# Performance work log

Measured on AMD Instinct MI355X. Metric: run time of the kernel, lower is better.

## Reference

```python
import jax, jax.numpy as jnp
import numpy as np

B, E, S, H = 4, 1024, 2048, 16  # batch, dim, seq_len, n_heads


def setup_inputs() -> dict:
    key = jax.random.key(0)
    ks = jax.random.split(key, 7)
    x = jax.random.normal(ks[0], (B, E, S), dtype=jnp.float32)
    in_w = jax.random.normal(ks[1], (E, E), dtype=jnp.float32) * (1.0 / np.sqrt(E))
    in_b = jnp.zeros((E,), dtype=jnp.float32)
    out_w = jax.random.normal(ks[2], (E, E), dtype=jnp.float32) * (1.0 / np.sqrt(E))
    out_b = jnp.zeros((E,), dtype=jnp.float32)
    mix_w = jax.random.normal(ks[3], (H, S), dtype=jnp.float32)
    mix_b = jnp.zeros((H, S), dtype=jnp.float32)
    return {"x": x, "in_w": in_w, "in_b": in_b, "out_w": out_w,
            "out_b": out_b, "mix_w": mix_w, "mix_b": mix_b}


def _head_matrices(mix_w):
    # First H/2 heads: column-repeat causal M[i,j] = v[j] if j >= i else 0.
    # Last  H/2 heads: row-repeat causal    M[i,j] = v[i] if j >= i else 0.
    idx = jnp.arange(S)
    mask = idx[None, :] >= idx[:, None]  # (S, S), True where j >= i
    Wcol = jnp.where(mask[None], mix_w[: H // 2, None, :], jnp.zeros((), mix_w.dtype))
    Wrow = jnp.where(mask[None], mix_w[H // 2 :, :, None], jnp.zeros((), mix_w.dtype))
    return jnp.concatenate([Wcol, Wrow], axis=0)  # (H, S, S)


def reference(x, in_w, in_b, out_w, out_b, mix_w, mix_b):
    e = E // H  # per-head channel dim
    xt = jnp.transpose(x, (0, 2, 1))           # b t e
    xt = xt @ in_w.T + in_b                    # in_proj
    # 'b t (h e) -> b h e t'
    p = jnp.transpose(xt.reshape(B, S, H, e), (0, 2, 3, 1))
    Wm = _head_matrices(mix_w)                 # (H, S, S)
    # bmm per (batch, head): (e, S) @ (S, S)
    out = jnp.einsum('bhet,hts->bhes', p, Wm) + mix_b[None, :, None, :]
    # 'b h e t -> b t (h e)'
    out = jnp.transpose(out, (0, 3, 1, 2)).reshape(B, S, E)
    out = out @ out_w.T + out_b                # out_proj
    return jnp.transpose(out, (0, 2, 1))       # b e t
```

## Files before the change

### kernel.cpp

```cpp
#include <hip/hip_runtime.h>

#define B_ 4
#define E_ 1024
#define S_ 2048
#define H_ 16
#define K_ 1024

#define NCH 32
#define CS  (S_/NCH)

typedef __bf16 bf16x8 __attribute__((ext_vector_type(8)));
typedef float  f32x4  __attribute__((ext_vector_type(4)));

#define AS1 __attribute__((address_space(1)))
#define AS3 __attribute__((address_space(3)))

__device__ __forceinline__ unsigned short f2bf(float f) {
  unsigned u = __float_as_uint(f);
  u += 0x7fffu + ((u >> 16) & 1u);
  return (unsigned short)(u >> 16);
}
__device__ __forceinline__ float bf2f(unsigned short h) {
  return __uint_as_float(((unsigned)h) << 16);
}

__global__ __launch_bounds__(256)
void tc_kernel(const float* __restrict__ x, unsigned short* __restrict__ xt,
               const float* __restrict__ inw, const float* __restrict__ outw,
               unsigned short* __restrict__ w1, unsigned short* __restrict__ w2)
{
  if (blockIdx.z == 4) {
    const int per = (E_ * E_) / 4;
    const int fid = blockIdx.y * 32 + blockIdx.x;
#pragma unroll
    for (int k = 0; k < 4; ++k) {
      int i = fid * 1024 + k * 256 + threadIdx.x;
      const float4* src = (i < per) ? (const float4*)inw : (const float4*)outw;
      unsigned short* dst = (i < per) ? w1 : w2;
      int j = (i < per) ? i : i - per;
      float4 v = src[j];
      ushort4 o;
      o.x = f2bf(v.x); o.y = f2bf(v.y); o.z = f2bf(v.z); o.w = f2bf(v.w);
      *(ushort4*)(dst + (long)j * 4) = o;
    }
    return;
  }

  __shared__ float t[64][65];
  const int b  = blockIdx.z;
  const int e0 = blockIdx.y * 64;
  const int s0 = blockIdx.x * 64;
  const int tx = threadIdx.x & 63, ty = threadIdx.x >> 6;

  const float* xp = x + ((long)b * E_ + e0) * S_ + s0;
#pragma unroll
  for (int r = 0; r < 16; ++r) {
    int row = r * 4 + ty;
    t[row][tx] = xp[(long)row * S_ + tx];
  }
  __syncthreads();
  unsigned short* xo = xt + ((long)b * S_ + s0) * E_ + e0;
#pragma unroll
  for (int p = 0; p < 2; ++p) {
    int s = p * 32 + (threadIdx.x >> 3);
    int e = (threadIdx.x & 7) * 8;
    unsigned short v[8];
#pragma unroll
    for (int j = 0; j < 8; ++j) v[j] = f2bf(t[e + j][s]);
    *(ushort4*)(xo + (long)s * E_ + e)     = make_ushort4(v[0], v[1], v[2], v[3]);
    *(ushort4*)(xo + (long)s * E_ + e + 4) = make_ushort4(v[4], v[5], v[6], v[7]);
  }
}

__device__ __forceinline__ void stage_half(char* lds, const unsigned short* __restrict__ base,
                                           int kt, int ks, int tid) {
  int row = tid >> 2;
  int cb  = (tid & 3) << 4;
  int cbs = cb ^ (((row >> 1) & 3) << 4);
  const unsigned short* src = base + (long)row * K_ + kt + ks * 32 + (cbs >> 1);
  __builtin_amdgcn_global_load_lds((const AS1 void*)src,
      (AS3 void*)(lds + ks * 8192 + tid * 16), 16, 0, 0);
}

__device__ __forceinline__ void stage_tile(char* buf, const unsigned short* __restrict__ Ab,
                                           const unsigned short* __restrict__ Bb,
                                           int kt, int tid) {
  stage_half(buf,         Ab, kt, 0, tid);
  stage_half(buf,         Ab, kt, 1, tid);
  stage_half(buf + 16384, Bb, kt, 0, tid);
  stage_half(buf + 16384, Bb, kt, 1, tid);
}

template<int VARIANT>
__global__ __launch_bounds__(512, 4)
void gemm_hw(const unsigned short* __restrict__ A, const unsigned short* __restrict__ Bw,
             void* __restrict__ Cout, const float* __restrict__ bias,
             const float* __restrict__ mixw, float* __restrict__ part)
{
  __shared__ char smem[65536];

  const int tid  = threadIdx.x;
  const int lane = tid & 63, wid = tid >> 6;
  const int wm = wid >> 2, wn = wid & 3;
  const int lr = lane & 15, lg = lane >> 4;

  const int bid = blockIdx.x;
  const int xcd = bid & 7;
  const int j   = bid >> 3;
  const int tm  = (xcd << 3) | (j & 7);
  const int tn  = j >> 3;

  const unsigned short* Ab = A  + (long)tm * 128 * K_;
  const unsigned short* Bb = Bw + (long)tn * 128 * K_;

  f32x4 acc[4][2] = {};

  stage_tile(smem, Ab, Bb, 0, tid);
  __syncthreads();

  for (int t = 0; t < 16; ++t) {
    char* cur = smem + (t & 1) * 32768;
    char* nxt = smem + ((t + 1) & 1) * 32768;
    if (t + 1 < 16) stage_tile(nxt, Ab, Bb, (t + 1) * 64, tid);

#pragma unroll
    for (int ks = 0; ks < 2; ++ks) {
      bf16x8 af[4], bfv[2];
#pragma unroll
      for (int mf = 0; mf < 4; ++mf) {
        int row = wm * 64 + mf * 16 + lr;
        int cb  = (lg * 16) ^ (((row >> 1) & 3) << 4);
        af[mf] = *(const bf16x8*)(cur + ks * 8192 + row * 64 + cb);
      }
#pragma unroll
      for (int nf = 0; nf < 2; ++nf) {
        int row = wn * 32 + nf * 16 + lr;
        int cb  = (lg * 16) ^ (((row >> 1) & 3) << 4);
        bfv[nf] = *(const bf16x8*)(cur + 16384 + ks * 8192 + row * 64 + cb);
      }
#pragma unroll
      for (int mf = 0; mf < 4; ++mf)
#pragma unroll
        for (int nf = 0; nf < 2; ++nf)
          acc[mf][nf] = __builtin_amdgcn_mfma_f32_16x16x32_bf16(
              af[mf], bfv[nf], acc[mf][nf], 0, 0, 0);
    }
    __syncthreads();
  }

  if constexpr (VARIANT == 0) {
    const int bt = tm >> 4;
    const int sb = ((tm & 15) << 7) + wm * 64;
    const int ch = ((tm & 15) << 1) + wm;
#pragma unroll
    for (int nf = 0; nf < 2; ++nf) {
      const int c = tn * 128 + wn * 32 + nf * 16 + lr;
      const float bv = bias[c];
      const int h = c >> 6;
      float sm = 0.f;
#pragma unroll
      for (int mf = 0; mf < 4; ++mf) {
#pragma unroll
        for (int jj = 0; jj < 4; ++jj) {
          const int sl = sb + mf * 16 + lg * 4 + jj;
          float v = acc[mf][nf][jj] + bv;
          ((unsigned short*)Cout)[((long)bt * S_ + sl) * E_ + c] = f2bf(v);
          sm += (h < 8) ? v : v * mixw[h * S_ + sl];
        }
      }
      sm += __shfl_xor(sm, 16, 64);
      sm += __shfl_xor(sm, 32, 64);
      if (lg == 0) part[((long)bt * NCH + ch) * E_ + c] = sm;
    }
  } else {
#pragma unroll
    for (int nf = 0; nf < 2; ++nf) {
      const int c = tn * 128 + wn * 32 + nf * 16 + lr;
      const float bv = bias[c];
#pragma unroll
      for (int mf = 0; mf < 4; ++mf) {
        const int r0 = tm * 128 + wm * 64 + mf * 16 + lg * 4;
        const int s = r0 & (S_ - 1);
        const int b = r0 >> 11;
        float4 v;
        v.x = acc[mf][nf][0] + bv; v.y = acc[mf][nf][1] + bv;
        v.z = acc[mf][nf][2] + bv; v.w = acc[mf][nf][3] + bv;
        *(float4*)((float*)Cout + ((long)b * E_ + c) * S_ + s) = v;
      }
    }
  }
}

__global__ __launch_bounds__(256)
void scan_final(const unsigned short* __restrict__ yt, const float* __restrict__ mixw,
                const float* __restrict__ mixb, const float* __restrict__ part,
                unsigned short* __restrict__ zt)
{
  const int b  = blockIdx.z;
  const int c  = blockIdx.y * 256 + threadIdx.x;
  const int ch = blockIdx.x;
  const int h  = c >> 6;
  float acc = 0.f;
  for (int p = 0; p < ch; ++p) acc += part[((long)b * NCH + p) * E_ + c];
  const unsigned short* yp = yt + ((long)b * S_ + ch * CS) * E_ + c;
  unsigned short*       zp = zt + ((long)b * S_ + ch * CS) * E_ + c;
  const float* mw = mixw + (long)h * S_ + ch * CS;
  const float* mb = mixb + (long)h * S_ + ch * CS;
  if (h < 8) {
    for (int s = 0; s < CS; ++s) {
      acc += bf2f(yp[(long)s * E_]);
      zp[(long)s * E_] = f2bf(fmaf(acc, mw[s], mb[s]));
    }
  } else {
    for (int s = 0; s < CS; ++s) {
      acc += bf2f(yp[(long)s * E_]) * mw[s];
      zp[(long)s * E_] = f2bf(acc + mb[s]);
    }
  }
}

extern "C" void kernel_launch(void* const* d_in, const int* in_sizes, int n_in,
                              void* d_out, int out_size, void* d_ws, size_t ws_size,
                              hipStream_t stream)
{
  (void)in_sizes; (void)n_in; (void)out_size; (void)ws_size;
  const float* x     = (const float*)d_in[0];
  const float* in_w  = (const float*)d_in[1];
  const float* in_b  = (const float*)d_in[2];
  const float* out_w = (const float*)d_in[3];
  const float* out_b = (const float*)d_in[4];
  const float* mix_w = (const float*)d_in[5];
  const float* mix_b = (const float*)d_in[6];

  char* ws = (char*)d_ws;
  unsigned short* Xt  = (unsigned short*)(ws);
  unsigned short* Yt  = (unsigned short*)(ws + (size_t)16 * 1024 * 1024);
  unsigned short* W1b = (unsigned short*)(ws + (size_t)32 * 1024 * 1024);
  unsigned short* W2b = (unsigned short*)(ws + (size_t)34 * 1024 * 1024);
  float*          part = (float*)(ws + (size_t)36 * 1024 * 1024);
  unsigned short* Zt  = Xt;

  tc_kernel<<<dim3(S_ / 64, E_ / 64, 5), 256, 0, stream>>>(x, Xt, in_w, out_w, W1b, W2b);

  gemm_hw<0><<<dim3(512), 512, 0, stream>>>(Xt, W1b, Yt, in_b, mix_w, part);

  scan_final<<<dim3(NCH, E_ / 256, B_), 256, 0, stream>>>(Yt, mix_w, mix_b, part, Zt);

  gemm_hw<1><<<dim3(512), 512, 0, stream>>>(Zt, W2b, d_out, out_b, nullptr, nullptr);
}
```

Before: 77.51 us.

## Fuse input transpose and fp32-to-bf16 conversion into GEMM tile staging

```diff
diff --git a/kernel.cpp b/kernel.cpp
--- a/kernel.cpp
+++ b/kernel.cpp
@@ -11,9 +11,11 @@
 
 typedef __bf16 bf16x8 __attribute__((ext_vector_type(8)));
 typedef float  f32x4  __attribute__((ext_vector_type(4)));
+typedef unsigned short u16x8 __attribute__((ext_vector_type(8)));
 
 #define AS1 __attribute__((address_space(1)))
 #define AS3 __attribute__((address_space(3)))
+#define SWZ(row) ((((row) >> 1) & 3) << 4)
 
 __device__ __forceinline__ unsigned short f2bf(float f) {
   unsigned u = __float_as_uint(f);
@@ -24,119 +26,92 @@
   return __uint_as_float(((unsigned)h) << 16);
 }
 
-__global__ __launch_bounds__(256)
-void tc_kernel(const float* __restrict__ x, unsigned short* __restrict__ xt,
-               const float* __restrict__ inw, const float* __restrict__ outw,
-               unsigned short* __restrict__ w1, unsigned short* __restrict__ w2)
-{
-  if (blockIdx.z == 4) {
-    const int per = (E_ * E_) / 4;
-    const int fid = blockIdx.y * 32 + blockIdx.x;
-#pragma unroll
-    for (int k = 0; k < 4; ++k) {
-      int i = fid * 1024 + k * 256 + threadIdx.x;
-      const float4* src = (i < per) ? (const float4*)inw : (const float4*)outw;
-      unsigned short* dst = (i < per) ? w1 : w2;
-      int j = (i < per) ? i : i - per;
-      float4 v = src[j];
-      ushort4 o;
-      o.x = f2bf(v.x); o.y = f2bf(v.y); o.z = f2bf(v.z); o.w = f2bf(v.w);
-      *(ushort4*)(dst + (long)j * 4) = o;
-    }
-    return;
-  }
-
-  __shared__ float t[64][65];
-  const int b  = blockIdx.z;
-  const int e0 = blockIdx.y * 64;
-  const int s0 = blockIdx.x * 64;
-  const int tx = threadIdx.x & 63, ty = threadIdx.x >> 6;
-
-  const float* xp = x + ((long)b * E_ + e0) * S_ + s0;
-#pragma unroll
-  for (int r = 0; r < 16; ++r) {
-    int row = r * 4 + ty;
-    t[row][tx] = xp[(long)row * S_ + tx];
-  }
-  __syncthreads();
-  unsigned short* xo = xt + ((long)b * S_ + s0) * E_ + e0;
-#pragma unroll
-  for (int p = 0; p < 2; ++p) {
-    int s = p * 32 + (threadIdx.x >> 3);
-    int e = (threadIdx.x & 7) * 8;
-    unsigned short v[8];
-#pragma unroll
-    for (int j = 0; j < 8; ++j) v[j] = f2bf(t[e + j][s]);
-    *(ushort4*)(xo + (long)s * E_ + e)     = make_ushort4(v[0], v[1], v[2], v[3]);
-    *(ushort4*)(xo + (long)s * E_ + e + 4) = make_ushort4(v[4], v[5], v[6], v[7]);
-  }
-}
-
-__device__ __forceinline__ void stage_half(char* lds, const unsigned short* __restrict__ base,
-                                           int kt, int ks, int tid) {
-  int row = tid >> 2;
-  int cb  = (tid & 3) << 4;
-  int cbs = cb ^ (((row >> 1) & 3) << 4);
-  const unsigned short* src = base + (long)row * K_ + kt + ks * 32 + (cbs >> 1);
-  __builtin_amdgcn_global_load_lds((const AS1 void*)src,
-      (AS3 void*)(lds + ks * 8192 + tid * 16), 16, 0, 0);
-}
-
-__device__ __forceinline__ void stage_tile(char* buf, const unsigned short* __restrict__ Ab,
-                                           const unsigned short* __restrict__ Bb,
-                                           int kt, int tid) {
-  stage_half(buf,         Ab, kt, 0, tid);
-  stage_half(buf,         Ab, kt, 1, tid);
-  stage_half(buf + 16384, Bb, kt, 0, tid);
-  stage_half(buf + 16384, Bb, kt, 1, tid);
-}
-
-template<int VARIANT>
 __global__ __launch_bounds__(512, 4)
-void gemm_hw(const unsigned short* __restrict__ A, const unsigned short* __restrict__ Bw,
-             void* __restrict__ Cout, const float* __restrict__ bias,
-             const float* __restrict__ mixw, float* __restrict__ part)
+void gemm1_fused(const float* __restrict__ x, const float* __restrict__ W1,
+                 unsigned short* __restrict__ Yt, const float* __restrict__ bias,
+                 const float* __restrict__ mixw, float* __restrict__ part)
 {
   __shared__ char smem[65536];
-
   const int tid  = threadIdx.x;
   const int lane = tid & 63, wid = tid >> 6;
   const int wm = wid >> 2, wn = wid & 3;
   const int lr = lane & 15, lg = lane >> 4;
 
   const int bid = blockIdx.x;
-  const int xcd = bid & 7;
-  const int j   = bid >> 3;
+  const int xcd = bid & 7, j = bid >> 3;
   const int tm  = (xcd << 3) | (j & 7);
   const int tn  = j >> 3;
 
-  const unsigned short* Ab = A  + (long)tm * 128 * K_;
-  const unsigned short* Bb = Bw + (long)tn * 128 * K_;
+  const int bt  = tm >> 4;
+  const int sl0 = (tm & 15) << 7;
+
+  const int ae  = tid & 63;
+  const int asq = tid >> 6;
+  const float* xbase = x + ((long)bt * E_ + ae) * S_ + sl0 + asq * 16;
+  const int bc  = tid >> 2;
+  const int beq = tid & 3;
+  const float* wbase = W1 + (long)(tn * 128 + bc) * E_ + beq * 16;
+
+  float4 ax[4], bx[4];
+  auto loadAB = [&](int t) {
+    const float* pa = xbase + (long)t * 64 * S_;
+    const float* pb = wbase + t * 64;
+#pragma unroll
+    for (int i = 0; i < 4; ++i) ax[i] = *(const float4*)(pa + i * 4);
+#pragma unroll
+    for (int i = 0; i < 4; ++i) bx[i] = *(const float4*)(pb + i * 4);
+  };
+  auto cvtwrite = [&](char* buf) {
+#pragma unroll
+    for (int i = 0; i < 4; ++i) {
+      float v0 = ax[i].x, v1 = ax[i].y, v2 = ax[i].z, v3 = ax[i].w;
+      int half = ae >> 5, colb = (ae & 31) * 2;
+#pragma unroll
+      for (int jj = 0; jj < 4; ++jj) {
+        int srow = asq * 16 + i * 4 + jj;
+        float vv = jj == 0 ? v0 : jj == 1 ? v1 : jj == 2 ? v2 : v3;
+        *(unsigned short*)(buf + half * 8192 + srow * 64 + (colb ^ SWZ(srow))) = f2bf(vv);
+      }
+    }
+    u16x8 bv[2];
+#pragma unroll
+    for (int i = 0; i < 4; ++i) {
+      bv[i >> 1][(i & 1) * 4 + 0] = f2bf(bx[i].x);
+      bv[i >> 1][(i & 1) * 4 + 1] = f2bf(bx[i].y);
+      bv[i >> 1][(i & 1) * 4 + 2] = f2bf(bx[i].z);
+      bv[i >> 1][(i & 1) * 4 + 3] = f2bf(bx[i].w);
+    }
+    int half = beq >> 1, colb = (beq & 1) * 32;
+    int base = 16384 + half * 8192 + bc * 64;
+#pragma unroll
+    for (int u = 0; u < 2; ++u)
+      *(u16x8*)(buf + base + ((colb + u * 16) ^ SWZ(bc))) = bv[u];
+  };
 
   f32x4 acc[4][2] = {};
 
-  stage_tile(smem, Ab, Bb, 0, tid);
+  loadAB(0);
+  cvtwrite(smem);
+  loadAB(1);
   __syncthreads();
 
   for (int t = 0; t < 16; ++t) {
     char* cur = smem + (t & 1) * 32768;
     char* nxt = smem + ((t + 1) & 1) * 32768;
-    if (t + 1 < 16) stage_tile(nxt, Ab, Bb, (t + 1) * 64, tid);
-
+    if (t < 15) cvtwrite(nxt);
+    if (t < 14) loadAB(t + 2);
 #pragma unroll
     for (int ks = 0; ks < 2; ++ks) {
       bf16x8 af[4], bfv[2];
 #pragma unroll
       for (int mf = 0; mf < 4; ++mf) {
         int row = wm * 64 + mf * 16 + lr;
-        int cb  = (lg * 16) ^ (((row >> 1) & 3) << 4);
-        af[mf] = *(const bf16x8*)(cur + ks * 8192 + row * 64 + cb);
+        af[mf] = *(const bf16x8*)(cur + ks * 8192 + row * 64 + ((lg * 16) ^ SWZ(row)));
       }
 #pragma unroll
       for (int nf = 0; nf < 2; ++nf) {
         int row = wn * 32 + nf * 16 + lr;
-        int cb  = (lg * 16) ^ (((row >> 1) & 3) << 4);
-        bfv[nf] = *(const bf16x8*)(cur + 16384 + ks * 8192 + row * 64 + cb);
+        bfv[nf] = *(const bf16x8*)(cur + 16384 + ks * 8192 + row * 64 + ((lg * 16) ^ SWZ(row)));
       }
 #pragma unroll
       for (int mf = 0; mf < 4; ++mf)
@@ -148,45 +123,136 @@
     __syncthreads();
   }
 
-  if constexpr (VARIANT == 0) {
-    const int bt = tm >> 4;
-    const int sb = ((tm & 15) << 7) + wm * 64;
-    const int ch = ((tm & 15) << 1) + wm;
-#pragma unroll
-    for (int nf = 0; nf < 2; ++nf) {
-      const int c = tn * 128 + wn * 32 + nf * 16 + lr;
-      const float bv = bias[c];
-      const int h = c >> 6;
-      float sm = 0.f;
+  const int sb = sl0 + wm * 64;
+  const int ch = ((tm & 15) << 1) + wm;
+#pragma unroll
+  for (int nf = 0; nf < 2; ++nf) {
+    const int c = tn * 128 + wn * 32 + nf * 16 + lr;
+    const float bv = bias[c];
+    const int h = c >> 6;
+    float sm = 0.f;
+#pragma unroll
+    for (int mf = 0; mf < 4; ++mf) {
+#pragma unroll
+      for (int jj = 0; jj < 4; ++jj) {
+        const int sl = sb + mf * 16 + lg * 4 + jj;
+        float v = acc[mf][nf][jj] + bv;
+        Yt[((long)bt * S_ + sl) * E_ + c] = f2bf(v);
+        sm += (h < 8) ? v : v * mixw[h * S_ + sl];
+      }
+    }
+    sm += __shfl_xor(sm, 16, 64);
+    sm += __shfl_xor(sm, 32, 64);
+    if (lg == 0) part[((long)bt * NCH + ch) * E_ + c] = sm;
+  }
+}
+
+__device__ __forceinline__ void stage_halfA(char* lds, const unsigned short* __restrict__ base,
+                                            int kt, int ks, int tid) {
+  int row = tid >> 2;
+  int cb  = (tid & 3) << 4;
+  int cbs = cb ^ SWZ(row);
+  const unsigned short* src = base + (long)row * K_ + kt + ks * 32 + (cbs >> 1);
+  __builtin_amdgcn_global_load_lds((const AS1 void*)src,
+      (AS3 void*)(lds + ks * 8192 + tid * 16), 16, 0, 0);
+}
+
+__global__ __launch_bounds__(512, 4)
+void gemm2_fused(const unsigned short* __restrict__ Zt, const float* __restrict__ W2,
+                 float* __restrict__ out, const float* __restrict__ bias)
+{
+  __shared__ char smem[65536];
+  const int tid  = threadIdx.x;
+  const int lane = tid & 63, wid = tid >> 6;
+  const int wm = wid >> 2, wn = wid & 3;
+  const int lr = lane & 15, lg = lane >> 4;
+
+  const int bid = blockIdx.x;
+  const int xcd = bid & 7, j = bid >> 3;
+  const int tm  = (xcd << 3) | (j & 7);
+  const int tn  = j >> 3;
+
+  const unsigned short* Ab = Zt + (long)tm * 128 * K_;
+  const int bc  = tid >> 2;
+  const int beq = tid & 3;
+  const float* wbase = W2 + (long)(tn * 128 + bc) * E_ + beq * 16;
+
+  float4 bx[4];
+  auto loadB = [&](int t) {
+    const float* pb = wbase + t * 64;
+#pragma unroll
+    for (int i = 0; i < 4; ++i) bx[i] = *(const float4*)(pb + i * 4);
+  };
+  auto cvtwriteB = [&](char* buf) {
+    u16x8 bv[2];
+#pragma unroll
+    for (int i = 0; i < 4; ++i) {
+      bv[i >> 1][(i & 1) * 4 + 0] = f2bf(bx[i].x);
+      bv[i >> 1][(i & 1) * 4 + 1] = f2bf(bx[i].y);
+      bv[i >> 1][(i & 1) * 4 + 2] = f2bf(bx[i].z);
+      bv[i >> 1][(i & 1) * 4 + 3] = f2bf(bx[i].w);
+    }
+    int half = beq >> 1, colb = (beq & 1) * 32;
+    int base = 16384 + half * 8192 + bc * 64;
+#pragma unroll
+    for (int u = 0; u < 2; ++u)
+      *(u16x8*)(buf + base + ((colb + u * 16) ^ SWZ(bc))) = bv[u];
+  };
+
+  f32x4 acc[4][2] = {};
+
+  loadB(0);
+  stage_halfA(smem, Ab, 0, 0, tid);
+  stage_halfA(smem, Ab, 0, 1, tid);
+  cvtwriteB(smem);
+  loadB(1);
+  __syncthreads();
+
+  for (int t = 0; t < 16; ++t) {
+    char* cur = smem + (t & 1) * 32768;
+    char* nxt = smem + ((t + 1) & 1) * 32768;
+    if (t < 15) {
+      stage_halfA(nxt, Ab, (t + 1) * 64, 0, tid);
+      stage_halfA(nxt, Ab, (t + 1) * 64, 1, tid);
+      cvtwriteB(nxt);
+    }
+    if (t < 14) loadB(t + 2);
+#pragma unroll
+    for (int ks = 0; ks < 2; ++ks) {
+      bf16x8 af[4], bfv[2];
 #pragma unroll
       for (int mf = 0; mf < 4; ++mf) {
-#pragma unroll
-        for (int jj = 0; jj < 4; ++jj) {
-          const int sl = sb + mf * 16 + lg * 4 + jj;
-          float v = acc[mf][nf][jj] + bv;
-          ((unsigned short*)Cout)[((long)bt * S_ + sl) * E_ + c] = f2bf(v);
-          sm += (h < 8) ? v : v * mixw[h * S_ + sl];
-        }
-      }
-      sm += __shfl_xor(sm, 16, 64);
-      sm += __shfl_xor(sm, 32, 64);
-      if (lg == 0) part[((long)bt * NCH + ch) * E_ + c] = sm;
-    }
-  } else {
-#pragma unroll
-    for (int nf = 0; nf < 2; ++nf) {
-      const int c = tn * 128 + wn * 32 + nf * 16 + lr;
-      const float bv = bias[c];
-#pragma unroll
-      for (int mf = 0; mf < 4; ++mf) {
-        const int r0 = tm * 128 + wm * 64 + mf * 16 + lg * 4;
-        const int s = r0 & (S_ - 1);
-        const int b = r0 >> 11;
-        float4 v;
-        v.x = acc[mf][nf][0] + bv; v.y = acc[mf][nf][1] + bv;
-        v.z = acc[mf][nf][2] + bv; v.w = acc[mf][nf][3] + bv;
-        *(float4*)((float*)Cout + ((long)b * E_ + c) * S_ + s) = v;
-      }
+        int row = wm * 64 + mf * 16 + lr;
+        af[mf] = *(const bf16x8*)(cur + ks * 8192 + row * 64 + ((lg * 16) ^ SWZ(row)));
+      }
+#pragma unroll
+      for (int nf = 0; nf < 2; ++nf) {
+        int row = wn * 32 + nf * 16 + lr;
+        bfv[nf] = *(const bf16x8*)(cur + 16384 + ks * 8192 + row * 64 + ((lg * 16) ^ SWZ(row)));
+      }
+#pragma unroll
+      for (int mf = 0; mf < 4; ++mf)
+#pragma unroll
+        for (int nf = 0; nf < 2; ++nf)
+          acc[mf][nf] = __builtin_amdgcn_mfma_f32_16x16x32_bf16(
+              af[mf], bfv[nf], acc[mf][nf], 0, 0, 0);
+    }
+    __syncthreads();
+  }
+
+#pragma unroll
+  for (int nf = 0; nf < 2; ++nf) {
+    const int c = tn * 128 + wn * 32 + nf * 16 + lr;
+    const float bv = bias[c];
+#pragma unroll
+    for (int mf = 0; mf < 4; ++mf) {
+      const int r0 = tm * 128 + wm * 64 + mf * 16 + lg * 4;
+      const int s = r0 & (S_ - 1);
+      const int b = r0 >> 11;
+      float4 v;
+      v.x = acc[mf][nf][0] + bv; v.y = acc[mf][nf][1] + bv;
+      v.z = acc[mf][nf][2] + bv; v.w = acc[mf][nf][3] + bv;
+      *(float4*)(out + ((long)b * E_ + c) * S_ + s) = v;
     }
   }
 }
@@ -233,18 +299,13 @@
   const float* mix_b = (const float*)d_in[6];
 
   char* ws = (char*)d_ws;
-  unsigned short* Xt  = (unsigned short*)(ws);
-  unsigned short* Yt  = (unsigned short*)(ws + (size_t)16 * 1024 * 1024);
-  unsigned short* W1b = (unsigned short*)(ws + (size_t)32 * 1024 * 1024);
-  unsigned short* W2b = (unsigned short*)(ws + (size_t)34 * 1024 * 1024);
-  float*          part = (float*)(ws + (size_t)36 * 1024 * 1024);
-  unsigned short* Zt  = Xt;
-
-  tc_kernel<<<dim3(S_ / 64, E_ / 64, 5), 256, 0, stream>>>(x, Xt, in_w, out_w, W1b, W2b);
-
-  gemm_hw<0><<<dim3(512), 512, 0, stream>>>(Xt, W1b, Yt, in_b, mix_w, part);
+  unsigned short* Yt  = (unsigned short*)(ws);
+  unsigned short* Zt  = (unsigned short*)(ws + (size_t)16 * 1024 * 1024);
+  float*          part = (float*)(ws + (size_t)32 * 1024 * 1024);
+
+  gemm1_fused<<<dim3(512), 512, 0, stream>>>(x, in_w, Yt, in_b, mix_w, part);
 
   scan_final<<<dim3(NCH, E_ / 256, B_), 256, 0, stream>>>(Yt, mix_w, mix_b, part, Zt);
 
-  gemm_hw<1><<<dim3(512), 512, 0, stream>>>(Zt, W2b, d_out, out_b, nullptr, nullptr);
-}
+  gemm2_fused<<<dim3(512), 512, 0, stream>>>(Zt, out_w, (float*)d_out, out_b);
+}
```

After: 109.3 us. +41.0%, slower.

## Fuse fp32 weight conversion into GEMM B staging and split K across warp pairs

Applied to the files above, without the earlier changes.

```diff
diff --git a/kernel.cpp b/kernel.cpp
--- a/kernel.cpp
+++ b/kernel.cpp
@@ -11,9 +11,11 @@
 
 typedef __bf16 bf16x8 __attribute__((ext_vector_type(8)));
 typedef float  f32x4  __attribute__((ext_vector_type(4)));
+typedef unsigned short u16x8 __attribute__((ext_vector_type(8)));
 
 #define AS1 __attribute__((address_space(1)))
 #define AS3 __attribute__((address_space(3)))
+#define SWZ(row) ((((row) >> 1) & 3) << 4)
 
 __device__ __forceinline__ unsigned short f2bf(float f) {
   unsigned u = __float_as_uint(f);
@@ -25,27 +27,8 @@
 }
 
 __global__ __launch_bounds__(256)
-void tc_kernel(const float* __restrict__ x, unsigned short* __restrict__ xt,
-               const float* __restrict__ inw, const float* __restrict__ outw,
-               unsigned short* __restrict__ w1, unsigned short* __restrict__ w2)
-{
-  if (blockIdx.z == 4) {
-    const int per = (E_ * E_) / 4;
-    const int fid = blockIdx.y * 32 + blockIdx.x;
-#pragma unroll
-    for (int k = 0; k < 4; ++k) {
-      int i = fid * 1024 + k * 256 + threadIdx.x;
-      const float4* src = (i < per) ? (const float4*)inw : (const float4*)outw;
-      unsigned short* dst = (i < per) ? w1 : w2;
-      int j = (i < per) ? i : i - per;
-      float4 v = src[j];
-      ushort4 o;
-      o.x = f2bf(v.x); o.y = f2bf(v.y); o.z = f2bf(v.z); o.w = f2bf(v.w);
-      *(ushort4*)(dst + (long)j * 4) = o;
-    }
-    return;
-  }
-
+void transpose_convert(const float* __restrict__ x, unsigned short* __restrict__ xt)
+{
   __shared__ float t[64][65];
   const int b  = blockIdx.z;
   const int e0 = blockIdx.y * 64;
@@ -72,120 +55,150 @@
   }
 }
 
-__device__ __forceinline__ void stage_half(char* lds, const unsigned short* __restrict__ base,
-                                           int kt, int ks, int tid) {
+__device__ __forceinline__ void stage_halfA(char* lds, const unsigned short* __restrict__ base,
+                                            int kt, int ks, int tid) {
   int row = tid >> 2;
   int cb  = (tid & 3) << 4;
-  int cbs = cb ^ (((row >> 1) & 3) << 4);
+  int cbs = cb ^ SWZ(row);
   const unsigned short* src = base + (long)row * K_ + kt + ks * 32 + (cbs >> 1);
   __builtin_amdgcn_global_load_lds((const AS1 void*)src,
       (AS3 void*)(lds + ks * 8192 + tid * 16), 16, 0, 0);
 }
 
-__device__ __forceinline__ void stage_tile(char* buf, const unsigned short* __restrict__ Ab,
-                                           const unsigned short* __restrict__ Bb,
-                                           int kt, int tid) {
-  stage_half(buf,         Ab, kt, 0, tid);
-  stage_half(buf,         Ab, kt, 1, tid);
-  stage_half(buf + 16384, Bb, kt, 0, tid);
-  stage_half(buf + 16384, Bb, kt, 1, tid);
-}
-
 template<int VARIANT>
 __global__ __launch_bounds__(512, 4)
-void gemm_hw(const unsigned short* __restrict__ A, const unsigned short* __restrict__ Bw,
+void gemm_ks(const unsigned short* __restrict__ A, const float* __restrict__ W,
              void* __restrict__ Cout, const float* __restrict__ bias,
              const float* __restrict__ mixw, float* __restrict__ part)
 {
   __shared__ char smem[65536];
-
   const int tid  = threadIdx.x;
   const int lane = tid & 63, wid = tid >> 6;
-  const int wm = wid >> 2, wn = wid & 3;
+  const int p  = wid >> 1, g = wid & 1;
+  const int wm = p >> 1,   wn = p & 1;
   const int lr = lane & 15, lg = lane >> 4;
 
   const int bid = blockIdx.x;
-  const int xcd = bid & 7;
-  const int j   = bid >> 3;
+  const int xcd = bid & 7, j = bid >> 3;
   const int tm  = (xcd << 3) | (j & 7);
   const int tn  = j >> 3;
 
-  const unsigned short* Ab = A  + (long)tm * 128 * K_;
-  const unsigned short* Bb = Bw + (long)tn * 128 * K_;
-
-  f32x4 acc[4][2] = {};
-
-  stage_tile(smem, Ab, Bb, 0, tid);
+  const unsigned short* Ab = A + (long)tm * 128 * K_;
+  const int bc  = tid >> 2;
+  const int beq = tid & 3;
+  const float* wbase = W + (long)(tn * 128 + bc) * E_ + beq * 16;
+
+  float4 bx[4];
+  auto loadB = [&](int t) {
+    const float* pb = wbase + t * 64;
+#pragma unroll
+    for (int i = 0; i < 4; ++i) bx[i] = *(const float4*)(pb + i * 4);
+  };
+  auto cvtwriteB = [&](char* buf) {
+    u16x8 bv[2];
+#pragma unroll
+    for (int i = 0; i < 4; ++i) {
+      bv[i >> 1][(i & 1) * 4 + 0] = f2bf(bx[i].x);
+      bv[i >> 1][(i & 1) * 4 + 1] = f2bf(bx[i].y);
+      bv[i >> 1][(i & 1) * 4 + 2] = f2bf(bx[i].z);
+      bv[i >> 1][(i & 1) * 4 + 3] = f2bf(bx[i].w);
+    }
+    int half = beq >> 1, colb = (beq & 1) * 32;
+    int base = 16384 + half * 8192 + bc * 64;
+#pragma unroll
+    for (int u = 0; u < 2; ++u)
+      *(u16x8*)(buf + base + ((colb + u * 16) ^ SWZ(bc))) = bv[u];
+  };
+
+  f32x4 acc[4][4] = {};
+
+  loadB(0);
+  stage_halfA(smem, Ab, 0, 0, tid);
+  stage_halfA(smem, Ab, 0, 1, tid);
+  cvtwriteB(smem);
+  loadB(1);
   __syncthreads();
 
   for (int t = 0; t < 16; ++t) {
     char* cur = smem + (t & 1) * 32768;
     char* nxt = smem + ((t + 1) & 1) * 32768;
-    if (t + 1 < 16) stage_tile(nxt, Ab, Bb, (t + 1) * 64, tid);
-
-#pragma unroll
-    for (int ks = 0; ks < 2; ++ks) {
-      bf16x8 af[4], bfv[2];
-#pragma unroll
-      for (int mf = 0; mf < 4; ++mf) {
-        int row = wm * 64 + mf * 16 + lr;
-        int cb  = (lg * 16) ^ (((row >> 1) & 3) << 4);
-        af[mf] = *(const bf16x8*)(cur + ks * 8192 + row * 64 + cb);
+    if (t < 15) {
+      stage_halfA(nxt, Ab, (t + 1) * 64, 0, tid);
+      stage_halfA(nxt, Ab, (t + 1) * 64, 1, tid);
+      cvtwriteB(nxt);
+    }
+    if (t < 14) loadB(t + 2);
+
+    bf16x8 af[4], bfv[4];
+#pragma unroll
+    for (int mf = 0; mf < 4; ++mf) {
+      int row = wm * 64 + mf * 16 + lr;
+      af[mf] = *(const bf16x8*)(cur + g * 8192 + row * 64 + ((lg * 16) ^ SWZ(row)));
+    }
+#pragma unroll
+    for (int nf = 0; nf < 4; ++nf) {
+      int row = wn * 64 + nf * 16 + lr;
+      bfv[nf] = *(const bf16x8*)(cur + 16384 + g * 8192 + row * 64 + ((lg * 16) ^ SWZ(row)));
+    }
+#pragma unroll
+    for (int mf = 0; mf < 4; ++mf)
+#pragma unroll
+      for (int nf = 0; nf < 4; ++nf)
+        acc[mf][nf] = __builtin_amdgcn_mfma_f32_16x16x32_bf16(
+            af[mf], bfv[nf], acc[mf][nf], 0, 0, 0);
+    __syncthreads();
+  }
+
+  f32x4* xch = (f32x4*)(void*)smem + p * 1024;
+  if (g == 1) {
+#pragma unroll
+    for (int i = 0; i < 16; ++i) xch[i * 64 + lane] = acc[i >> 2][i & 3];
+  }
+  __syncthreads();
+  if (g == 0) {
+#pragma unroll
+    for (int i = 0; i < 16; ++i) acc[i >> 2][i & 3] += xch[i * 64 + lane];
+
+    if constexpr (VARIANT == 0) {
+      const int bt  = tm >> 4;
+      const int sl0 = (tm & 15) << 7;
+      const int sb  = sl0 + wm * 64;
+      const int ch  = ((tm & 15) << 1) + wm;
+#pragma unroll
+      for (int nf = 0; nf < 4; ++nf) {
+        const int c = tn * 128 + wn * 64 + nf * 16 + lr;
+        const float bv = bias[c];
+        const int h = c >> 6;
+        float sm = 0.f;
+#pragma unroll
+        for (int mf = 0; mf < 4; ++mf) {
+#pragma unroll
+          for (int jj = 0; jj < 4; ++jj) {
+            const int sl = sb + mf * 16 + lg * 4 + jj;
+            float v = acc[mf][nf][jj] + bv;
+            ((unsigned short*)Cout)[((long)bt * S_ + sl) * E_ + c] = f2bf(v);
+            sm += (h < 8) ? v : v * mixw[h * S_ + sl];
+          }
+        }
+        sm += __shfl_xor(sm, 16, 64);
+        sm += __shfl_xor(sm, 32, 64);
+        if (lg == 0) part[((long)bt * NCH + ch) * E_ + c] = sm;
       }
-#pragma unroll
-      for (int nf = 0; nf < 2; ++nf) {
-        int row = wn * 32 + nf * 16 + lr;
-        int cb  = (lg * 16) ^ (((row >> 1) & 3) << 4);
-        bfv[nf] = *(const bf16x8*)(cur + 16384 + ks * 8192 + row * 64 + cb);
-      }
-#pragma unroll
-      for (int mf = 0; mf < 4; ++mf)
-#pragma unroll
-        for (int nf = 0; nf < 2; ++nf)
-          acc[mf][nf] = __builtin_amdgcn_mfma_f32_16x16x32_bf16(
-              af[mf], bfv[nf], acc[mf][nf], 0, 0, 0);
-    }
-    __syncthreads();
-  }
-
-  if constexpr (VARIANT == 0) {
-    const int bt = tm >> 4;
-    const int sb = ((tm & 15) << 7) + wm * 64;
-    const int ch = ((tm & 15) << 1) + wm;
-#pragma unroll
-    for (int nf = 0; nf < 2; ++nf) {
-      const int c = tn * 128 + wn * 32 + nf * 16 + lr;
-      const float bv = bias[c];
-      const int h = c >> 6;
-      float sm = 0.f;
-#pragma unroll
-      for (int mf = 0; mf < 4; ++mf) {
-#pragma unroll
-        for (int jj = 0; jj < 4; ++jj) {
-          const int sl = sb + mf * 16 + lg * 4 + jj;
-          float v = acc[mf][nf][jj] + bv;
-          ((unsigned short*)Cout)[((long)bt * S_ + sl) * E_ + c] = f2bf(v);
-          sm += (h < 8) ? v : v * mixw[h * S_ + sl];
+    } else {
+#pragma unroll
+      for (int nf = 0; nf < 4; ++nf) {
+        const int c = tn * 128 + wn * 64 + nf * 16 + lr;
+        const float bv = bias[c];
+#pragma unroll
+        for (int mf = 0; mf < 4; ++mf) {
+          const int r0 = tm * 128 + wm * 64 + mf * 16 + lg * 4;
+          const int s = r0 & (S_ - 1);
+          const int b = r0 >> 11;
+          float4 v;
+          v.x = acc[mf][nf][0] + bv; v.y = acc[mf][nf][1] + bv;
+          v.z = acc[mf][nf][2] + bv; v.w = acc[mf][nf][3] + bv;
+          *(float4*)((float*)Cout + ((long)b * E_ + c) * S_ + s) = v;
         }
-      }
-      sm += __shfl_xor(sm, 16, 64);
-      sm += __shfl_xor(sm, 32, 64);
-      if (lg == 0) part[((long)bt * NCH + ch) * E_ + c] = sm;
-    }
-  } else {
-#pragma unroll
-    for (int nf = 0; nf < 2; ++nf) {
-      const int c = tn * 128 + wn * 32 + nf * 16 + lr;
-      const float bv = bias[c];
-#pragma unroll
-      for (int mf = 0; mf < 4; ++mf) {
-        const int r0 = tm * 128 + wm * 64 + mf * 16 + lg * 4;
-        const int s = r0 & (S_ - 1);
-        const int b = r0 >> 11;
-        float4 v;
-        v.x = acc[mf][nf][0] + bv; v.y = acc[mf][nf][1] + bv;
-        v.z = acc[mf][nf][2] + bv; v.w = acc[mf][nf][3] + bv;
-        *(float4*)((float*)Cout + ((long)b * E_ + c) * S_ + s) = v;
       }
     }
   }
@@ -235,16 +248,14 @@
   char* ws = (char*)d_ws;
   unsigned short* Xt  = (unsigned short*)(ws);
   unsigned short* Yt  = (unsigned short*)(ws + (size_t)16 * 1024 * 1024);
-  unsigned short* W1b = (unsigned short*)(ws + (size_t)32 * 1024 * 1024);
-  unsigned short* W2b = (unsigned short*)(ws + (size_t)34 * 1024 * 1024);
-  float*          part = (float*)(ws + (size_t)36 * 1024 * 1024);
+  float*          part = (float*)(ws + (size_t)32 * 1024 * 1024);
   unsigned short* Zt  = Xt;
 
-  tc_kernel<<<dim3(S_ / 64, E_ / 64, 5), 256, 0, stream>>>(x, Xt, in_w, out_w, W1b, W2b);
-
-  gemm_hw<0><<<dim3(512), 512, 0, stream>>>(Xt, W1b, Yt, in_b, mix_w, part);
+  transpose_convert<<<dim3(S_ / 64, E_ / 64, B_), 256, 0, stream>>>(x, Xt);
+
+  gemm_ks<0><<<dim3(512), 512, 0, stream>>>(Xt, in_w, Yt, in_b, mix_w, part);
 
   scan_final<<<dim3(NCH, E_ / 256, B_), 256, 0, stream>>>(Yt, mix_w, mix_b, part, Zt);
 
-  gemm_hw<1><<<dim3(512), 512, 0, stream>>>(Zt, W2b, d_out, out_b, nullptr, nullptr);
-}
+  gemm_ks<1><<<dim3(512), 512, 0, stream>>>(Zt, out_w, d_out, out_b, nullptr, nullptr);
+}
```

After: 121.9 us. 1.57x slower.

## Enlarge GEMM block tile to 256x128 with 1024 threads

Applied to the files above, without the earlier changes.

```diff
diff --git a/kernel.cpp b/kernel.cpp
--- a/kernel.cpp
+++ b/kernel.cpp
@@ -14,6 +14,7 @@
 
 #define AS1 __attribute__((address_space(1)))
 #define AS3 __attribute__((address_space(3)))
+#define SWZ(row) ((((row) >> 1) & 3) << 4)
 
 __device__ __forceinline__ unsigned short f2bf(float f) {
   unsigned u = __float_as_uint(f);
@@ -72,45 +73,49 @@
   }
 }
 
-__device__ __forceinline__ void stage_half(char* lds, const unsigned short* __restrict__ base,
-                                           int kt, int ks, int tid) {
-  int row = tid >> 2;
-  int cb  = (tid & 3) << 4;
-  int cbs = cb ^ (((row >> 1) & 3) << 4);
-  const unsigned short* src = base + (long)row * K_ + kt + ks * 32 + (cbs >> 1);
-  __builtin_amdgcn_global_load_lds((const AS1 void*)src,
-      (AS3 void*)(lds + ks * 8192 + tid * 16), 16, 0, 0);
-}
+#define BB1 49152
 
 __device__ __forceinline__ void stage_tile(char* buf, const unsigned short* __restrict__ Ab,
                                            const unsigned short* __restrict__ Bb,
                                            int kt, int tid) {
-  stage_half(buf,         Ab, kt, 0, tid);
-  stage_half(buf,         Ab, kt, 1, tid);
-  stage_half(buf + 16384, Bb, kt, 0, tid);
-  stage_half(buf + 16384, Bb, kt, 1, tid);
+#pragma unroll
+  for (int i = 0; i < 2; ++i) {
+    int row = tid >> 2;
+    int cb  = (tid & 3) << 4;
+    int cbs = cb ^ SWZ(row);
+    const unsigned short* src = Ab + (long)row * K_ + kt + i * 32 + (cbs >> 1);
+    __builtin_amdgcn_global_load_lds((const AS1 void*)src,
+        (AS3 void*)(buf + i * 16384 + tid * 16), 16, 0, 0);
+  }
+  {
+    int ks  = tid >> 9;
+    int row = (tid >> 2) & 127;
+    int cb  = (tid & 3) << 4;
+    int cbs = cb ^ SWZ(row);
+    const unsigned short* src = Bb + (long)row * K_ + kt + ks * 32 + (cbs >> 1);
+    __builtin_amdgcn_global_load_lds((const AS1 void*)src,
+        (AS3 void*)(buf + 32768 + tid * 16), 16, 0, 0);
+  }
 }
 
 template<int VARIANT>
-__global__ __launch_bounds__(512, 4)
-void gemm_hw(const unsigned short* __restrict__ A, const unsigned short* __restrict__ Bw,
-             void* __restrict__ Cout, const float* __restrict__ bias,
-             const float* __restrict__ mixw, float* __restrict__ part)
-{
-  __shared__ char smem[65536];
-
+__global__ __launch_bounds__(1024, 4)
+void gemm_big(const unsigned short* __restrict__ A, const unsigned short* __restrict__ Bw,
+              void* __restrict__ Cout, const float* __restrict__ bias,
+              const float* __restrict__ mixw, float* __restrict__ part)
+{
+  extern __shared__ char smem[];
   const int tid  = threadIdx.x;
   const int lane = tid & 63, wid = tid >> 6;
   const int wm = wid >> 2, wn = wid & 3;
   const int lr = lane & 15, lg = lane >> 4;
 
   const int bid = blockIdx.x;
-  const int xcd = bid & 7;
-  const int j   = bid >> 3;
-  const int tm  = (xcd << 3) | (j & 7);
-  const int tn  = j >> 3;
-
-  const unsigned short* Ab = A  + (long)tm * 128 * K_;
+  const int xcd = bid & 7, j = bid >> 3;
+  const int tm  = (xcd << 2) | (j & 3);
+  const int tn  = j >> 2;
+
+  const unsigned short* Ab = A  + (long)tm * 256 * K_;
   const unsigned short* Bb = Bw + (long)tn * 128 * K_;
 
   f32x4 acc[4][2] = {};
@@ -119,8 +124,8 @@
   __syncthreads();
 
   for (int t = 0; t < 16; ++t) {
-    char* cur = smem + (t & 1) * 32768;
-    char* nxt = smem + ((t + 1) & 1) * 32768;
+    char* cur = smem + (t & 1) * BB1;
+    char* nxt = smem + ((t + 1) & 1) * BB1;
     if (t + 1 < 16) stage_tile(nxt, Ab, Bb, (t + 1) * 64, tid);
 
 #pragma unroll
@@ -129,14 +134,12 @@
 #pragma unroll
       for (int mf = 0; mf < 4; ++mf) {
         int row = wm * 64 + mf * 16 + lr;
-        int cb  = (lg * 16) ^ (((row >> 1) & 3) << 4);
-        af[mf] = *(const bf16x8*)(cur + ks * 8192 + row * 64 + cb);
+        af[mf] = *(const bf16x8*)(cur + ks * 16384 + row * 64 + ((lg * 16) ^ SWZ(row)));
       }
 #pragma unroll
       for (int nf = 0; nf < 2; ++nf) {
         int row = wn * 32 + nf * 16 + lr;
-        int cb  = (lg * 16) ^ (((row >> 1) & 3) << 4);
-        bfv[nf] = *(const bf16x8*)(cur + 16384 + ks * 8192 + row * 64 + cb);
+        bfv[nf] = *(const bf16x8*)(cur + 32768 + ks * 8192 + row * 64 + ((lg * 16) ^ SWZ(row)));
       }
 #pragma unroll
       for (int mf = 0; mf < 4; ++mf)
@@ -149,9 +152,10 @@
   }
 
   if constexpr (VARIANT == 0) {
-    const int bt = tm >> 4;
-    const int sb = ((tm & 15) << 7) + wm * 64;
-    const int ch = ((tm & 15) << 1) + wm;
+    const int bt  = tm >> 3;
+    const int sl0 = (tm & 7) << 8;
+    const int sb  = sl0 + wm * 64;
+    const int ch  = ((tm & 7) << 2) + wm;
 #pragma unroll
     for (int nf = 0; nf < 2; ++nf) {
       const int c = tn * 128 + wn * 32 + nf * 16 + lr;
@@ -179,7 +183,7 @@
       const float bv = bias[c];
 #pragma unroll
       for (int mf = 0; mf < 4; ++mf) {
-        const int r0 = tm * 128 + wm * 64 + mf * 16 + lg * 4;
+        const int r0 = tm * 256 + wm * 64 + mf * 16 + lg * 4;
         const int s = r0 & (S_ - 1);
         const int b = r0 >> 11;
         float4 v;
@@ -240,11 +244,14 @@
   float*          part = (float*)(ws + (size_t)36 * 1024 * 1024);
   unsigned short* Zt  = Xt;
 
+  hipFuncSetAttribute((const void*)gemm_big<0>, hipFuncAttributeMaxDynamicSharedMemorySize, 98304);
+  hipFuncSetAttribute((const void*)gemm_big<1>, hipFuncAttributeMaxDynamicSharedMemorySize, 98304);
+
   tc_kernel<<<dim3(S_ / 64, E_ / 64, 5), 256, 0, stream>>>(x, Xt, in_w, out_w, W1b, W2b);
 
-  gemm_hw<0><<<dim3(512), 512, 0, stream>>>(Xt, W1b, Yt, in_b, mix_w, part);
+  gemm_big<0><<<dim3(256), 1024, 98304, stream>>>(Xt, W1b, Yt, in_b, mix_w, part);
 
   scan_final<<<dim3(NCH, E_ / 256, B_), 256, 0, stream>>>(Yt, mix_w, mix_b, part, Zt);
 
-  gemm_hw<1><<<dim3(512), 512, 0, stream>>>(Zt, W2b, d_out, out_b, nullptr, nullptr);
-}
+  gemm_big<1><<<dim3(256), 1024, 98304, stream>>>(Zt, W2b, d_out, out_b, nullptr, nullptr);
+}
```

New measurement: 82.30 us. 6.2% more time.
